# Optimization experiments

Hardware: AMD Instinct MI355X
Metric: run time of the kernel (lower is better)

Reference implementation:

```python
import jax, jax.numpy as jnp
import numpy as np

# global prototype index ranges per scale: scale s owns protos [s0, s1)
SCALES = ((0, 100), (100, 200))
NEG = jnp.float32(-1e30)


def _scale_terms(d, lab_flat, cls_of):
    """d: [B,P,Hs,Ws] distances for this scale; lab_flat: [B,N] downsampled labels
    (already shifted by -1); cls_of: [P] class id of each local prototype.
    Returns (sum of exp(-sym_kld) over valid prototype pairs, number of valid pairs).
    """
    B, P = d.shape[0], d.shape[1]
    dflat = d.reshape(B, P, -1)                                   # [B,P,N]
    M = lab_flat[:, None, :] == cls_of[None, :, None]             # [B,P,N] pixel mask per proto's class
    count = M.sum(-1)                                             # [B,P] masked pixel count
    # masked log_softmax over the class pixels of each prototype
    lse = jax.nn.logsumexp(jnp.where(M, dflat, NEG), axis=-1)     # [B,P]
    L = jnp.where(M, dflat - lse[:, :, None], 0.0)                # log-probs on mask, 0 elsewhere
    Pr = jnp.where(M, jnp.exp(L), 0.0)                            # probs on mask, 0 elsewhere
    E = jnp.sum(Pr * L, axis=-1)                                  # [B,P] sum p*log p
    # Cmat[b,a,c] = sum_n Pr[b,a,n] * L[b,c,n]
    Cmat = jnp.einsum('ban,bcn->bac', Pr, L)                      # [B,P,P]
    # sym_kld[b,j,k] = 0.5*((E_k - sum p_k log p_j) + (E_j - sum p_j log p_k))
    kld = 0.5 * (E[:, None, :] + E[:, :, None] - Cmat - jnp.swapaxes(Cmat, 1, 2))
    idx = jnp.arange(P)
    same = (cls_of[:, None] == cls_of[None, :]) & (idx[:, None] < idx[None, :])  # j<k, same class
    valid = same[None] & (count[:, :, None] >= 2) & (count[:, None, :] >= 2)      # need >=2 masked pixels
    return jnp.sum(jnp.where(valid, jnp.exp(-kld), 0.0)), jnp.sum(valid)


def reference(dist0, dist1, target_labels, proto_class):
    lab = target_labels - 1                                       # [B,H,W], -1 = ignore
    B, H, W = lab.shape
    tot = jnp.float32(0.0)
    cnt = jnp.int32(0)
    for d, (s0, s1) in zip((dist0, dist1), SCALES):
        Hs, Ws = d.shape[2], d.shape[3]
        # torch F.interpolate(mode='nearest'): src index = floor(dst * in/out)
        ri = (jnp.arange(Hs) * H) // Hs
        ci = (jnp.arange(Ws) * W) // Ws
        lab_flat = lab[:, ri][:, :, ci].reshape(B, Hs * Ws)
        s, n = _scale_terms(d, lab_flat, proto_class[s0:s1])
        tot = tot + s
        cnt = cnt + n
    return jnp.where(cnt > 0, tot / jnp.maximum(cnt, 1).astype(jnp.float32), jnp.float32(0.0))


def setup_inputs() -> dict:
    key = jax.random.key(0)
    k0, k1, k2 = jax.random.split(key, 3)
    B, C, PPC = 16, 20, 5  # batch, num classes, protos per class per scale
    dist0 = jax.random.normal(k0, (B, 100, 128, 128), dtype=jnp.float32)
    dist1 = jax.random.normal(k1, (B, 100, 64, 64), dtype=jnp.float32)
    # labels in 1..C ; 0 becomes -1 after the shift and is ignored
    target_labels = jax.random.randint(k2, (B, 512, 512), 0, C + 1).astype(jnp.int32)
    proto_class = ((jnp.arange(200) % 100) // PPC).astype(jnp.int32)
    return {"dist0": dist0, "dist1": dist1, "target_labels": target_labels, "proto_class": proto_class}
```

## Files before the change

### kernel.cpp

```cpp
#include <hip/hip_runtime.h>
#include <math.h>

#define TPB 256
#define NCLS 20
#define PPC 5
#define NB 16
#define N0 16384
#define N1 4096
#define RECSZ 36
#define NBLKA 1600
#define NBLKB 640

__global__ void downsample_labels(const int* __restrict__ tgt,
                                  char* __restrict__ lab0, char* __restrict__ lab1) {
    const int q = blockIdx.x * blockDim.x + threadIdx.x;
    if (q < 65536) {
        const int b = q >> 12, r = q & 4095;
        const int i = r >> 5, j0 = (r & 31) << 2;
        const int* src = tgt + b * 262144 + (i << 2) * 512;
        char4 v;
        v.x = (char)(src[(j0 + 0) << 2] - 1);
        v.y = (char)(src[(j0 + 1) << 2] - 1);
        v.z = (char)(src[(j0 + 2) << 2] - 1);
        v.w = (char)(src[(j0 + 3) << 2] - 1);
        ((char4*)lab0)[q] = v;
    } else {
        const int k = q - 65536;
        const int b = k >> 10, r = k & 1023;
        const int i = r >> 4, j0 = (r & 15) << 2;
        const int* src = tgt + b * 262144 + (i << 3) * 512;
        char4 v;
        v.x = (char)(src[(j0 + 0) << 3] - 1);
        v.y = (char)(src[(j0 + 1) << 3] - 1);
        v.z = (char)(src[(j0 + 2) << 3] - 1);
        v.w = (char)(src[(j0 + 3) << 3] - 1);
        ((char4*)lab1)[k] = v;
    }
}

__global__ __launch_bounds__(TPB, 2) void kA(const float* __restrict__ dist0,
                                             const float* __restrict__ dist1,
                                             const char* __restrict__ lab0,
                                             const char* __restrict__ lab1,
                                             float* __restrict__ recs) {
    const int blk = blockIdx.x;
    int scale, bc, split;
    if (blk < 1280) { scale = 0; bc = blk >> 2; split = blk & 3; }
    else            { scale = 1; bc = blk - 1280; split = 0; }
    const int b = bc / NCLS, c = bc % NCLS;
    const int N = scale ? N1 : N0;
    const float* dist = scale ? dist1 : dist0;
    const char* lab = (scale ? lab1 + b * N1 : lab0 + b * N0) + split * 4096;

    const int tid = threadIdx.x, lane = tid & 63, w = tid >> 6;
    const char4* lab4 = (const char4*)lab;
    const float* base = dist + (size_t)(b * 100 + c * PPC) * N + split * 4096;

    float4 A[4][PPC];
    char4 L[4];
#pragma unroll
    for (int it = 0; it < 4; ++it) {
        const int idx4 = w * 256 + it * 64 + lane;
        L[it] = lab4[idx4];
#pragma unroll
        for (int p = 0; p < PPC; ++p)
            A[it][p] = ((const float4*)(base + (size_t)p * N))[idx4];
    }

    float m[PPC], s[PPC], T1[PPC * PPC];
#pragma unroll
    for (int p = 0; p < PPC; ++p) { m[p] = -INFINITY; s[p] = 0.f; }
#pragma unroll
    for (int i = 0; i < PPC * PPC; ++i) T1[i] = 0.f;
    int kcnt = 0;

#pragma unroll
    for (int it = 0; it < 4; ++it) {
#define DO_E(F)                                                                     \
        if ((int)L[it].F == c) {                                                    \
            float dv[PPC] = {A[it][0].F, A[it][1].F, A[it][2].F,                    \
                             A[it][3].F, A[it][4].F};                               \
            _Pragma("unroll")                                                       \
            for (int p = 0; p < PPC; ++p) {                                         \
                const float nm = fmaxf(m[p], dv[p]);                                \
                const float f  = __expf(m[p] - nm);           \
                const float e  = __expf(dv[p] - nm);                                \
                m[p] = nm;                                                          \
                s[p] = s[p] * f + e;                                                \
                _Pragma("unroll")                                                   \
                for (int bb = 0; bb < PPC; ++bb)                                    \
                    T1[p * PPC + bb] = T1[p * PPC + bb] * f + e * dv[bb];           \
            }                                                                       \
            ++kcnt;                                                                 \
        }
        DO_E(x) DO_E(y) DO_E(z) DO_E(w)
#undef DO_E
    }

    float M[PPC];
#pragma unroll
    for (int p = 0; p < PPC; ++p) M[p] = m[p];
#pragma unroll
    for (int d = 32; d >= 1; d >>= 1)
#pragma unroll
        for (int p = 0; p < PPC; ++p) M[p] = fmaxf(M[p], __shfl_xor(M[p], d, 64));

#pragma unroll
    for (int p = 0; p < PPC; ++p) {
        const float f = (m[p] == -INFINITY) ? 0.f : __expf(m[p] - M[p]);
        s[p] *= f;
#pragma unroll
        for (int bb = 0; bb < PPC; ++bb) T1[p * PPC + bb] *= f;
    }
    float kc = (float)kcnt;
#pragma unroll
    for (int d = 32; d >= 1; d >>= 1) {
#pragma unroll
        for (int p = 0; p < PPC; ++p) s[p] += __shfl_xor(s[p], d, 64);
#pragma unroll
        for (int i = 0; i < PPC * PPC; ++i) T1[i] += __shfl_xor(T1[i], d, 64);
        kc += __shfl_xor(kc, d, 64);
    }

    if (lane == 0) {
        float* r = recs + (size_t)(blk * 4 + w) * RECSZ;
#pragma unroll
        for (int p = 0; p < PPC; ++p) { r[p] = M[p]; r[PPC + p] = s[p]; }
#pragma unroll
        for (int i = 0; i < PPC * PPC; ++i) r[10 + i] = T1[i];
        r[35] = kc;
    }
}

__global__ __launch_bounds__(64) void kB(const float* __restrict__ recs,
                                         float* __restrict__ psum,
                                         float* __restrict__ pcnt) {
    const int blk = blockIdx.x;
    const int lane = threadIdx.x;
    const int scale = (blk >= 320) ? 1 : 0;
    const int bc = blk - scale * 320;
    const int rbase = scale ? (5120 + bc * 4) : (bc * 16);
    const int nrec = scale ? 4 : 16;
    const int a = (lane < 25) ? lane / 5 : 0;
    const int bb = (lane < 25) ? lane % 5 : 0;

    float M = -INFINITY, cnt = 0.f;
    if (lane < 5)
        for (int r = 0; r < nrec; ++r)
            M = fmaxf(M, recs[(size_t)(rbase + r) * RECSZ + lane]);
    if (lane == 0)
        for (int r = 0; r < nrec; ++r)
            cnt += recs[(size_t)(rbase + r) * RECSZ + 35];
    cnt = __shfl(cnt, 0, 64);

    float S = 0.f;
    if (lane < 5)
        for (int r = 0; r < nrec; ++r) {
            const float* rr = recs + (size_t)(rbase + r) * RECSZ;
            S += rr[5 + lane] * expf(rr[lane] - M);
        }
    float lse = 0.f;
    if (lane < 5) lse = M + logf(S);

    const float Ma    = __shfl(M, a, 64);
    const float Sa    = __shfl(S, a, 64);
    const float lse_b = __shfl(lse, bb, 64);

    float U = 0.f;
    if (lane < 25)
        for (int r = 0; r < nrec; ++r) {
            const float* rr = recs + (size_t)(rbase + r) * RECSZ;
            U += rr[10 + lane] * expf(rr[a] - Ma);
        }
    const float C = U / Sa - lse_b;

    float tot = 0.f;
#pragma unroll
    for (int j = 0; j < PPC; ++j)
#pragma unroll
        for (int k = j + 1; k < PPC; ++k) {
            const float Ejj = __shfl(C, j * 5 + j, 64);
            const float Ekk = __shfl(C, k * 5 + k, 64);
            const float Cjk = __shfl(C, j * 5 + k, 64);
            const float Ckj = __shfl(C, k * 5 + j, 64);
            tot += expf(-0.5f * (Ejj + Ekk - Cjk - Ckj));
        }
    if (lane == 0) {
        const bool ok = (cnt >= 2.f);
        psum[blk] = ok ? tot : 0.f;
        pcnt[blk] = ok ? 10.f : 0.f;
    }
}

__global__ void finalize_kernel(const float* __restrict__ psum,
                                const float* __restrict__ pcnt,
                                float* __restrict__ out) {
    __shared__ float rs[TPB], rc[TPB];
    const int tid = threadIdx.x;
    float s = 0.f, c = 0.f;
    for (int i = tid; i < NBLKB; i += TPB) { s += psum[i]; c += pcnt[i]; }
    rs[tid] = s; rc[tid] = c;
    __syncthreads();
    for (int off = 128; off > 0; off >>= 1) {
        if (tid < off) { rs[tid] += rs[tid + off]; rc[tid] += rc[tid + off]; }
        __syncthreads();
    }
    if (tid == 0) out[0] = (rc[0] > 0.f) ? (rs[0] / rc[0]) : 0.f;
}

extern "C" void kernel_launch(void* const* d_in, const int* in_sizes, int n_in,
                              void* d_out, int out_size, void* d_ws, size_t ws_size,
                              hipStream_t stream) {
    const float* dist0 = (const float*)d_in[0];
    const float* dist1 = (const float*)d_in[1];
    const int*   tgt   = (const int*)d_in[2];
    float* out = (float*)d_out;

    char*  lab0 = (char*)d_ws;
    char*  lab1 = lab0 + 262144;
    float* recs = (float*)(lab0 + 327680);
    float* psum = recs + (size_t)NBLKA * 4 * RECSZ;
    float* pcnt = psum + NBLKB;

    downsample_labels<<<320, TPB, 0, stream>>>(tgt, lab0, lab1);
    kA<<<NBLKA, TPB, 0, stream>>>(dist0, dist1, lab0, lab1, recs);
    kB<<<NBLKB, 64, 0, stream>>>(recs, psum, pcnt);
    finalize_kernel<<<1, TPB, 0, stream>>>(psum, pcnt, out);
}
```

Baseline: 51.56 us.

## Use two-pass max-then-exp softmax stats, halve per-block work, merge wave records in-block

After: 55.46 us. 7.6% more time.

```diff
diff --git a/kernel.cpp b/kernel.cpp
--- a/kernel.cpp
+++ b/kernel.cpp
@@ -8,7 +8,7 @@
 #define N0 16384
 #define N1 4096
 #define RECSZ 36
-#define NBLKA 1600
+#define NBLKA 3200
 #define NBLKB 640
 
 __global__ void downsample_labels(const int* __restrict__ tgt,
@@ -38,80 +38,77 @@
     }
 }
 
-__global__ __launch_bounds__(TPB, 2) void kA(const float* __restrict__ dist0,
+__global__ __launch_bounds__(TPB, 4) void kA(const float* __restrict__ dist0,
                                              const float* __restrict__ dist1,
                                              const char* __restrict__ lab0,
                                              const char* __restrict__ lab1,
                                              float* __restrict__ recs) {
+    __shared__ float wrec[4][RECSZ];
+
     const int blk = blockIdx.x;
     int scale, bc, split;
-    if (blk < 1280) { scale = 0; bc = blk >> 2; split = blk & 3; }
-    else            { scale = 1; bc = blk - 1280; split = 0; }
+    if (blk < 2560) { scale = 0; bc = blk >> 3; split = blk & 7; }
+    else            { const int k = blk - 2560; scale = 1; bc = k >> 1; split = k & 1; }
     const int b = bc / NCLS, c = bc % NCLS;
     const int N = scale ? N1 : N0;
     const float* dist = scale ? dist1 : dist0;
-    const char* lab = (scale ? lab1 + b * N1 : lab0 + b * N0) + split * 4096;
+    const char* lab = (scale ? lab1 + b * N1 : lab0 + b * N0) + split * 2048;
+    const float* base = dist + (size_t)(b * 100 + c * PPC) * N + split * 2048;
+    const char4* lab4 = (const char4*)lab;
 
     const int tid = threadIdx.x, lane = tid & 63, w = tid >> 6;
-    const char4* lab4 = (const char4*)lab;
-    const float* base = dist + (size_t)(b * 100 + c * PPC) * N + split * 4096;
-
-    float4 A[4][PPC];
-    char4 L[4];
-#pragma unroll
-    for (int it = 0; it < 4; ++it) {
-        const int idx4 = w * 256 + it * 64 + lane;
+
+    float4 A[2][PPC];
+    char4 L[2];
+#pragma unroll
+    for (int it = 0; it < 2; ++it) {
+        const int idx4 = w * 128 + it * 64 + lane;
         L[it] = lab4[idx4];
 #pragma unroll
         for (int p = 0; p < PPC; ++p)
             A[it][p] = ((const float4*)(base + (size_t)p * N))[idx4];
     }
 
-    float m[PPC], s[PPC], T1[PPC * PPC];
-#pragma unroll
-    for (int p = 0; p < PPC; ++p) { m[p] = -INFINITY; s[p] = 0.f; }
+    float M[PPC];
+#pragma unroll
+    for (int p = 0; p < PPC; ++p) M[p] = -INFINITY;
+    int kcnt = 0;
+#pragma unroll
+    for (int it = 0; it < 2; ++it) {
+#define PH1(F) if ((int)L[it].F == c) {                                   \
+            M[0] = fmaxf(M[0], A[it][0].F); M[1] = fmaxf(M[1], A[it][1].F); \
+            M[2] = fmaxf(M[2], A[it][2].F); M[3] = fmaxf(M[3], A[it][3].F); \
+            M[4] = fmaxf(M[4], A[it][4].F); ++kcnt; }
+        PH1(x) PH1(y) PH1(z) PH1(w)
+#undef PH1
+    }
+#pragma unroll
+    for (int d = 32; d >= 1; d >>= 1)
+#pragma unroll
+        for (int p = 0; p < PPC; ++p) M[p] = fmaxf(M[p], __shfl_xor(M[p], d, 64));
+
+    float s[PPC], T1[PPC * PPC];
+#pragma unroll
+    for (int p = 0; p < PPC; ++p) s[p] = 0.f;
 #pragma unroll
     for (int i = 0; i < PPC * PPC; ++i) T1[i] = 0.f;
-    int kcnt = 0;
-
-#pragma unroll
-    for (int it = 0; it < 4; ++it) {
-#define DO_E(F)                                                                     \
-        if ((int)L[it].F == c) {                                                    \
-            float dv[PPC] = {A[it][0].F, A[it][1].F, A[it][2].F,                    \
-                             A[it][3].F, A[it][4].F};                               \
-            _Pragma("unroll")                                                       \
-            for (int p = 0; p < PPC; ++p) {                                         \
-                const float nm = fmaxf(m[p], dv[p]);                                \
-                const float f  = __expf(m[p] - nm);           \
-                const float e  = __expf(dv[p] - nm);                                \
-                m[p] = nm;                                                          \
-                s[p] = s[p] * f + e;                                                \
-                _Pragma("unroll")                                                   \
-                for (int bb = 0; bb < PPC; ++bb)                                    \
-                    T1[p * PPC + bb] = T1[p * PPC + bb] * f + e * dv[bb];           \
-            }                                                                       \
-            ++kcnt;                                                                 \
-        }
-        DO_E(x) DO_E(y) DO_E(z) DO_E(w)
-#undef DO_E
-    }
-
-    float M[PPC];
-#pragma unroll
-    for (int p = 0; p < PPC; ++p) M[p] = m[p];
-#pragma unroll
-    for (int d = 32; d >= 1; d >>= 1)
-#pragma unroll
-        for (int p = 0; p < PPC; ++p) M[p] = fmaxf(M[p], __shfl_xor(M[p], d, 64));
-
-#pragma unroll
-    for (int p = 0; p < PPC; ++p) {
-        const float f = (m[p] == -INFINITY) ? 0.f : __expf(m[p] - M[p]);
-        s[p] *= f;
-#pragma unroll
-        for (int bb = 0; bb < PPC; ++bb) T1[p * PPC + bb] *= f;
-    }
+#pragma unroll
+    for (int it = 0; it < 2; ++it) {
+#define PH2(F) if ((int)L[it].F == c) {                                              \
+            float dv[PPC] = {A[it][0].F, A[it][1].F, A[it][2].F, A[it][3].F,         \
+                             A[it][4].F};                                            \
+            float e[PPC];                                                            \
+            _Pragma("unroll")                                                        \
+            for (int p = 0; p < PPC; ++p) { e[p] = __expf(dv[p] - M[p]); s[p] += e[p]; } \
+            _Pragma("unroll")                                                        \
+            for (int aa = 0; aa < PPC; ++aa)                                         \
+            _Pragma("unroll")                                                        \
+                for (int bb = 0; bb < PPC; ++bb)                                     \
+                    T1[aa * PPC + bb] = fmaf(e[aa], dv[bb], T1[aa * PPC + bb]); }
+        PH2(x) PH2(y) PH2(z) PH2(w)
+#undef PH2
+    }
+
     float kc = (float)kcnt;
 #pragma unroll
     for (int d = 32; d >= 1; d >>= 1) {
@@ -123,12 +120,43 @@
     }
 
     if (lane == 0) {
-        float* r = recs + (size_t)(blk * 4 + w) * RECSZ;
-#pragma unroll
-        for (int p = 0; p < PPC; ++p) { r[p] = M[p]; r[PPC + p] = s[p]; }
-#pragma unroll
-        for (int i = 0; i < PPC * PPC; ++i) r[10 + i] = T1[i];
-        r[35] = kc;
+#pragma unroll
+        for (int p = 0; p < PPC; ++p) { wrec[w][p] = M[p]; wrec[w][PPC + p] = s[p]; }
+#pragma unroll
+        for (int i = 0; i < PPC * PPC; ++i) wrec[w][10 + i] = T1[i];
+        wrec[w][35] = kc;
+    }
+    __syncthreads();
+
+    if (w == 0) {
+        float* r = recs + (size_t)blk * RECSZ;
+        if (lane < 25) {
+            const int a = lane / 5;
+            const float Mb = fmaxf(fmaxf(wrec[0][a], wrec[1][a]),
+                                   fmaxf(wrec[2][a], wrec[3][a]));
+            float acc = 0.f;
+#pragma unroll
+            for (int wi = 0; wi < 4; ++wi) {
+                const float mw = wrec[wi][a];
+                const float f = (mw == -INFINITY) ? 0.f : __expf(mw - Mb);
+                acc += wrec[wi][10 + lane] * f;
+            }
+            r[10 + lane] = acc;
+        } else if (lane < 30) {
+            const int p = lane - 25;
+            const float Mb = fmaxf(fmaxf(wrec[0][p], wrec[1][p]),
+                                   fmaxf(wrec[2][p], wrec[3][p]));
+            float acc = 0.f;
+#pragma unroll
+            for (int wi = 0; wi < 4; ++wi) {
+                const float mw = wrec[wi][p];
+                const float f = (mw == -INFINITY) ? 0.f : __expf(mw - Mb);
+                acc += wrec[wi][5 + p] * f;
+            }
+            r[p] = Mb; r[5 + p] = acc;
+        } else if (lane == 30) {
+            r[35] = wrec[0][35] + wrec[1][35] + wrec[2][35] + wrec[3][35];
+        }
     }
 }
 
@@ -139,8 +167,8 @@
     const int lane = threadIdx.x;
     const int scale = (blk >= 320) ? 1 : 0;
     const int bc = blk - scale * 320;
-    const int rbase = scale ? (5120 + bc * 4) : (bc * 16);
-    const int nrec = scale ? 4 : 16;
+    const int rbase = scale ? (2560 + bc * 2) : (bc * 8);
+    const int nrec = scale ? 2 : 8;
     const int a = (lane < 25) ? lane / 5 : 0;
     const int bb = (lane < 25) ? lane % 5 : 0;
 
@@ -219,7 +247,7 @@
     char*  lab0 = (char*)d_ws;
     char*  lab1 = lab0 + 262144;
     float* recs = (float*)(lab0 + 327680);
-    float* psum = recs + (size_t)NBLKA * 4 * RECSZ;
+    float* psum = recs + (size_t)NBLKA * RECSZ;
     float* pcnt = psum + NBLKB;
 
     downsample_labels<<<320, TPB, 0, stream>>>(tgt, lab0, lab1);
```

## Drop online max tracking in softmax stats and use single-wave software-pipelined blocks

Applied to the files above, without the earlier changes.

Measured after the change: 43.86 us. 1.18x faster.

```diff
diff --git a/kernel.cpp b/kernel.cpp
--- a/kernel.cpp
+++ b/kernel.cpp
@@ -7,8 +7,8 @@
 #define NB 16
 #define N0 16384
 #define N1 4096
-#define RECSZ 36
-#define NBLKA 1600
+#define RECSZ 32
+#define NWA 3200
 #define NBLKB 640
 
 __global__ void downsample_labels(const int* __restrict__ tgt,
@@ -38,97 +38,82 @@
     }
 }
 
-__global__ __launch_bounds__(TPB, 2) void kA(const float* __restrict__ dist0,
-                                             const float* __restrict__ dist1,
-                                             const char* __restrict__ lab0,
-                                             const char* __restrict__ lab1,
-                                             float* __restrict__ recs) {
+__global__ __launch_bounds__(64) void kA(const float* __restrict__ dist0,
+                                         const float* __restrict__ dist1,
+                                         const char* __restrict__ lab0,
+                                         const char* __restrict__ lab1,
+                                         float* __restrict__ recs) {
     const int blk = blockIdx.x;
-    int scale, bc, split;
-    if (blk < 1280) { scale = 0; bc = blk >> 2; split = blk & 3; }
-    else            { scale = 1; bc = blk - 1280; split = 0; }
+    int scale, bc, seg;
+    if (blk < 2560) { scale = 0; bc = blk >> 3; seg = blk & 7; }
+    else            { const int k = blk - 2560; scale = 1; bc = k >> 1; seg = k & 1; }
     const int b = bc / NCLS, c = bc % NCLS;
     const int N = scale ? N1 : N0;
     const float* dist = scale ? dist1 : dist0;
-    const char* lab = (scale ? lab1 + b * N1 : lab0 + b * N0) + split * 4096;
+    const char* lab = (scale ? lab1 + b * N1 : lab0 + b * N0) + seg * 2048;
+    const float* base = dist + (size_t)(b * 100 + c * PPC) * N + seg * 2048;
 
-    const int tid = threadIdx.x, lane = tid & 63, w = tid >> 6;
+    const int lane = threadIdx.x;
+    const float4* r0 = (const float4*)(base);
+    const float4* r1 = (const float4*)(base + N);
+    const float4* r2 = (const float4*)(base + 2 * N);
+    const float4* r3 = (const float4*)(base + 3 * N);
+    const float4* r4 = (const float4*)(base + 4 * N);
     const char4* lab4 = (const char4*)lab;
-    const float* base = dist + (size_t)(b * 100 + c * PPC) * N + split * 4096;
 
-    float4 A[4][PPC];
-    char4 L[4];
+    float s[PPC] = {0.f, 0.f, 0.f, 0.f, 0.f};
+    float T1[25];
 #pragma unroll
-    for (int it = 0; it < 4; ++it) {
-        const int idx4 = w * 256 + it * 64 + lane;
-        L[it] = lab4[idx4];
-#pragma unroll
-        for (int p = 0; p < PPC; ++p)
-            A[it][p] = ((const float4*)(base + (size_t)p * N))[idx4];
-    }
-
-    float m[PPC], s[PPC], T1[PPC * PPC];
-#pragma unroll
-    for (int p = 0; p < PPC; ++p) { m[p] = -INFINITY; s[p] = 0.f; }
-#pragma unroll
-    for (int i = 0; i < PPC * PPC; ++i) T1[i] = 0.f;
+    for (int i = 0; i < 25; ++i) T1[i] = 0.f;
     int kcnt = 0;
 
+    char4 L = lab4[lane];
+    float4 A0 = r0[lane], A1 = r1[lane], A2 = r2[lane], A3 = r3[lane], A4 = r4[lane];
+
 #pragma unroll
-    for (int it = 0; it < 4; ++it) {
-#define DO_E(F)                                                                     \
-        if ((int)L[it].F == c) {                                                    \
-            float dv[PPC] = {A[it][0].F, A[it][1].F, A[it][2].F,                    \
-                             A[it][3].F, A[it][4].F};                               \
-            _Pragma("unroll")                                                       \
-            for (int p = 0; p < PPC; ++p) {                                         \
-                const float nm = fmaxf(m[p], dv[p]);                                \
-                const float f  = __expf(m[p] - nm);           \
-                const float e  = __expf(dv[p] - nm);                                \
-                m[p] = nm;                                                          \
-                s[p] = s[p] * f + e;                                                \
-                _Pragma("unroll")                                                   \
-                for (int bb = 0; bb < PPC; ++bb)                                    \
-                    T1[p * PPC + bb] = T1[p * PPC + bb] * f + e * dv[bb];           \
-            }                                                                       \
-            ++kcnt;                                                                 \
+    for (int it = 0; it < 8; ++it) {
+        char4 Ln;
+        float4 B0, B1, B2, B3, B4;
+        if (it < 7) {
+            const int ni = (it + 1) * 64 + lane;
+            Ln = lab4[ni];
+            B0 = r0[ni]; B1 = r1[ni]; B2 = r2[ni]; B3 = r3[ni]; B4 = r4[ni];
+        }
+#define DO_E(F)                                                                  \
+        if ((int)L.F == c) {                                                     \
+            float dv[PPC] = {A0.F, A1.F, A2.F, A3.F, A4.F};                      \
+            float ev[PPC];                                                       \
+            _Pragma("unroll")                                                    \
+            for (int p = 0; p < PPC; ++p) { ev[p] = __expf(dv[p]); s[p] += ev[p]; } \
+            _Pragma("unroll")                                                    \
+            for (int aa = 0; aa < PPC; ++aa)                                     \
+            _Pragma("unroll")                                                    \
+                for (int bb = 0; bb < PPC; ++bb)                                 \
+                    T1[aa * PPC + bb] = fmaf(ev[aa], dv[bb], T1[aa * PPC + bb]); \
+            ++kcnt;                                                              \
         }
         DO_E(x) DO_E(y) DO_E(z) DO_E(w)
 #undef DO_E
+        L = Ln; A0 = B0; A1 = B1; A2 = B2; A3 = B3; A4 = B4;
     }
 
-    float M[PPC];
-#pragma unroll
-    for (int p = 0; p < PPC; ++p) M[p] = m[p];
-#pragma unroll
-    for (int d = 32; d >= 1; d >>= 1)
-#pragma unroll
-        for (int p = 0; p < PPC; ++p) M[p] = fmaxf(M[p], __shfl_xor(M[p], d, 64));
-
-#pragma unroll
-    for (int p = 0; p < PPC; ++p) {
-        const float f = (m[p] == -INFINITY) ? 0.f : __expf(m[p] - M[p]);
-        s[p] *= f;
-#pragma unroll
-        for (int bb = 0; bb < PPC; ++bb) T1[p * PPC + bb] *= f;
-    }
     float kc = (float)kcnt;
 #pragma unroll
     for (int d = 32; d >= 1; d >>= 1) {
 #pragma unroll
         for (int p = 0; p < PPC; ++p) s[p] += __shfl_xor(s[p], d, 64);
 #pragma unroll
-        for (int i = 0; i < PPC * PPC; ++i) T1[i] += __shfl_xor(T1[i], d, 64);
+        for (int i = 0; i < 25; ++i) T1[i] += __shfl_xor(T1[i], d, 64);
         kc += __shfl_xor(kc, d, 64);
     }
 
     if (lane == 0) {
-        float* r = recs + (size_t)(blk * 4 + w) * RECSZ;
+        float* r = recs + (size_t)blk * RECSZ;
 #pragma unroll
-        for (int p = 0; p < PPC; ++p) { r[p] = M[p]; r[PPC + p] = s[p]; }
+        for (int p = 0; p < PPC; ++p) r[p] = s[p];
 #pragma unroll
-        for (int i = 0; i < PPC * PPC; ++i) r[10 + i] = T1[i];
-        r[35] = kc;
+        for (int i = 0; i < 25; ++i) r[5 + i] = T1[i];
+        r[30] = kc;
     }
 }
 
@@ -139,39 +124,23 @@
     const int lane = threadIdx.x;
     const int scale = (blk >= 320) ? 1 : 0;
     const int bc = blk - scale * 320;
-    const int rbase = scale ? (5120 + bc * 4) : (bc * 16);
-    const int nrec = scale ? 4 : 16;
+    const int rbase = scale ? (2560 + bc * 2) : (bc * 8);
+    const int nrec = scale ? 2 : 8;
     const int a = (lane < 25) ? lane / 5 : 0;
     const int bb = (lane < 25) ? lane % 5 : 0;
 
-    float M = -INFINITY, cnt = 0.f;
+    float S = 0.f, U = 0.f, cnt = 0.f;
     if (lane < 5)
-        for (int r = 0; r < nrec; ++r)
-            M = fmaxf(M, recs[(size_t)(rbase + r) * RECSZ + lane]);
+        for (int r = 0; r < nrec; ++r) S += recs[(size_t)(rbase + r) * RECSZ + lane];
+    if (lane < 25)
+        for (int r = 0; r < nrec; ++r) U += recs[(size_t)(rbase + r) * RECSZ + 5 + lane];
     if (lane == 0)
-        for (int r = 0; r < nrec; ++r)
-            cnt += recs[(size_t)(rbase + r) * RECSZ + 35];
+        for (int r = 0; r < nrec; ++r) cnt += recs[(size_t)(rbase + r) * RECSZ + 30];
     cnt = __shfl(cnt, 0, 64);
 
-    float S = 0.f;
-    if (lane < 5)
-        for (int r = 0; r < nrec; ++r) {
-            const float* rr = recs + (size_t)(rbase + r) * RECSZ;
-            S += rr[5 + lane] * expf(rr[lane] - M);
-        }
-    float lse = 0.f;
-    if (lane < 5) lse = M + logf(S);
-
-    const float Ma    = __shfl(M, a, 64);
+    const float lse = (lane < 5) ? logf(S) : 0.f;
     const float Sa    = __shfl(S, a, 64);
     const float lse_b = __shfl(lse, bb, 64);
-
-    float U = 0.f;
-    if (lane < 25)
-        for (int r = 0; r < nrec; ++r) {
-            const float* rr = recs + (size_t)(rbase + r) * RECSZ;
-            U += rr[10 + lane] * expf(rr[a] - Ma);
-        }
     const float C = U / Sa - lse_b;
 
     float tot = 0.f;
@@ -219,11 +188,11 @@
     char*  lab0 = (char*)d_ws;
     char*  lab1 = lab0 + 262144;
     float* recs = (float*)(lab0 + 327680);
-    float* psum = recs + (size_t)NBLKA * 4 * RECSZ;
+    float* psum = recs + (size_t)NWA * RECSZ;
     float* pcnt = psum + NBLKB;
 
     downsample_labels<<<320, TPB, 0, stream>>>(tgt, lab0, lab1);
-    kA<<<NBLKA, TPB, 0, stream>>>(dist0, dist1, lab0, lab1, recs);
+    kA<<<NWA, 64, 0, stream>>>(dist0, dist1, lab0, lab1, recs);
     kB<<<NBLKB, 64, 0, stream>>>(recs, psum, pcnt);
     finalize_kernel<<<1, TPB, 0, stream>>>(psum, pcnt, out);
 }
```
